# Performance work log

Hardware: AMD Instinct MI355X
Metric: run time of the kernel (lower is better)

The kernel has to match this reference:

```python
import jax, jax.numpy as jnp
import numpy as np

B, CIN, N, K, G, COUT = 8, 128, 2048, 16, 4, 256
NL = COUT // 4          # nl_channels = int(0.25*out_channels) = 64
L = COUT - NL           # l_channels = 192
CL = L // G             # 48 per local head
CNL = NL // G           # 16 per non-local head


def setup_inputs() -> dict:
    key = jax.random.key(0)
    ks = jax.random.split(key, 16)
    s = 0.05
    r = lambda k_, sh: s * jax.random.normal(k_, sh, jnp.float32)
    return {
        "x": jax.random.normal(ks[0], (B, CIN, N, K), jnp.float32),
        "abs_x": jax.random.normal(ks[1], (B, CIN // 2, N, 1), jnp.float32),
        "points": jax.random.normal(ks[2], (B, 3, N), jnp.float32),
        "Wq": r(ks[3], (L, CIN // 2)),
        "Wk": r(ks[4], (L, CIN // 2)),
        "Wv": r(ks[5], (L, CIN)),
        "Wnq": r(ks[6], (NL, CIN // 2)),
        "Wnk": r(ks[7], (NL, CIN // 2)),
        "Wnv1": r(ks[8], (NL, CIN // 2)),
        "Wnv2": r(ks[9], (NL, CIN // 2)),
        "pe_w1": r(ks[10], (3, L)),
        "pe_b1": jnp.zeros((L,), jnp.float32),
        "pe_w2": r(ks[11], (L, L)),
        "pe_b2": jnp.zeros((L,), jnp.float32),
        "npe_w1": r(ks[12], (G, 3, CNL)),
        "npe_b1": jnp.zeros((G, CNL), jnp.float32),
        "npe_w2": r(ks[13], (G, CNL, CNL)),
        "npe_b2": jnp.zeros((G, CNL), jnp.float32),
        "idx": jax.random.randint(ks[14], (B, 1, N, K), 0, N, dtype=jnp.int32),
    }


def _forward(x, abs_x, points, Wq, Wk, Wv, Wnq, Wnk, Wnv1, Wnv2,
             pe_w1, pe_b1, pe_w2, pe_b2, npe_w1, npe_b1, npe_w2, npe_b2, idx):
    b, c, n, k = x.shape
    half = c // 2
    idx_sq = idx[:, 0]                                   # (b,n,k)

    # ---- 1. Local attention over kNN neighbors ----
    lq = jnp.einsum('oc,bcns->bons', Wq, abs_x).reshape(b, G, CL, n, 1)
    lk = jnp.einsum('oc,bcnk->bonk', Wk, x[:, half:] + x[:, :half]).reshape(b, G, CL, n, k)
    lv = jnp.einsum('oc,bcnk->bonk', Wv, x).reshape(b, G, CL, n, k)

    # absolute positional encoding (select_neighbors -> carte MLP)
    nbr = jax.vmap(lambda p, i: p[:, i])(points, idx_sq)  # (b,3,n,k)
    rel = nbr - nbr[..., 0:1]                             # subtract first neighbor
    h = jax.nn.relu(jnp.einsum('bcnk,cd->bnkd', rel, pe_w1) + pe_b1)
    pe = (jnp.einsum('bnkd,de->bnke', h, pe_w2) + pe_b2).transpose(0, 3, 1, 2)
    lk = lk + pe.reshape(b, G, CL, n, k)

    att = jax.nn.softmax((lq * lk).sum(2), axis=-1)       # (b,G,n,k)
    local_feature = jnp.einsum('bgnk,bgcnk->bgcn', att, lv).reshape(b, L, n, 1)

    # ---- scatter-based sparse attention centrality + top-k node selection ----
    idx_flat = idx_sq.reshape(b, n * k)
    att_flat = att.reshape(b, G, n * k)

    def scat(a_g, i):  # a_g: (G, n*k), i: (n*k,)
        return jax.vmap(lambda a: jnp.zeros((n,), a.dtype).at[i].add(a))(a_g)

    cent = jax.vmap(scat)(att_flat, idx_flat)             # (b,G,n)
    vals, inds = jax.lax.top_k(cent, k)                   # (b,G,k)

    # ---- 2. Non-local MHA over selected nodes ----
    a2 = abs_x[..., 0]                                    # (b,half,n)
    nq = jnp.einsum('oc,bcn->bon', Wnq, a2).reshape(b, G, CNL, n)
    nk_ = jnp.einsum('oc,bcn->bon', Wnk, a2).reshape(b, G, CNL, n)
    nv1 = jnp.einsum('oc,bcn->bon', Wnv1, a2).reshape(b, G, CNL, n)
    nv2 = jnp.einsum('oc,bcn->bon', Wnv2, a2).reshape(b, G, CNL, n)

    gi = inds[:, :, None, :]                              # (b,G,1,k)
    nk_sel = jnp.take_along_axis(nk_, gi, axis=3)         # (b,G,CNL,k)
    nv2j = jnp.take_along_axis(nv2, gi, axis=3)           # (b,G,CNL,k)

    # per-group non-local positional encoding (constant over n by construction)
    sel = jnp.take_along_axis(jnp.broadcast_to(points[:, None], (b, G, 3, n)), gi, axis=3)  # (b,G,3,k)
    rel_nl = sel - sel[..., 0:1]
    h2 = jax.nn.relu(jnp.einsum('bgck,gcd->bgkd', rel_nl, npe_w1) + npe_b1[None, :, None, :])
    pe_nl = (jnp.einsum('bgkd,gde->bgke', h2, npe_w2) + npe_b2[None, :, None, :]).transpose(0, 1, 3, 2)  # (b,G,CNL,k)

    att_nl = jax.nn.softmax(jnp.einsum('bgcn,bgck->bgnk', nq, nk_sel + pe_nl), axis=-1)
    # value[b,g,c,n,k] = nv1[...,n] - nv2[...,n] + nv2j[...,k], gated by tanh(centrality)
    w = att_nl * jnp.tanh(vals)[:, :, None, :]            # (b,G,n,k)
    s = w.sum(-1)                                         # (b,G,n)
    nl_feature = (nv1 - nv2) * s[:, :, None, :] + jnp.einsum('bgnk,bgck->bgcn', w, nv2j)
    nl_feature = nl_feature.reshape(b, NL, n, 1)

    return jnp.concatenate([local_feature, nl_feature], axis=1)  # (b,COUT,n,1)


def reference(x, abs_x, points, Wq, Wk, Wv, Wnq, Wnk, Wnv1, Wnv2,
              pe_w1, pe_b1, pe_w2, pe_b2, npe_w1, npe_b1, npe_w2, npe_b2, idx):
    return _forward(x, abs_x, points, Wq, Wk, Wv, Wnq, Wnk, Wnv1, Wnv2,
                    pe_w1, pe_b1, pe_w2, pe_b2, npe_w1, npe_b1, npe_w2, npe_b2, idx)
```

## Files before the change

kernel.cpp:

```cpp
#include <hip/hip_runtime.h>
#include <cstddef>

constexpr int NN = 2048;
constexpr int GG = 4;

__global__ __launch_bounds__(256) void prep_q(const float* __restrict__ Wq,
                                              const float* __restrict__ Wk,
                                              const float* __restrict__ pe_w2,
                                              float* __restrict__ Qbuf) {
    const int g = blockIdx.x >> 6, c2 = blockIdx.x & 63;
    const int row = threadIdx.x;
    float acc = 0.f;
    if (row < 64) {
        for (int j = 0; j < 48; ++j) {
            const int o = g * 48 + j;
            acc = fmaf(Wk[o * 64 + row], Wq[o * 64 + c2], acc);
        }
    } else {
        const int d = row - 64;
        for (int j = 0; j < 48; ++j) {
            const int o = g * 48 + j;
            acc = fmaf(pe_w2[(size_t)d * 192 + o], Wq[o * 64 + c2], acc);
        }
    }
    Qbuf[((size_t)(g * 64 + c2) << 8) + row] = acc;
}

__global__ __launch_bounds__(256, 4) void local_v5(
    const float* __restrict__ x, const float* __restrict__ abs_x,
    const float* __restrict__ points, const float* __restrict__ Wv,
    const float* __restrict__ pe_w1, const float* __restrict__ pe_b1,
    const int* __restrict__ idx, const float* __restrict__ Qbuf,
    float* __restrict__ out, float* __restrict__ cent)
{
    const int bn = blockIdx.x;
    const int b  = bn >> 9;
    const int n0 = (bn & 511) << 2;
    const int tid = threadIdx.x;

    __shared__ int   sidx[64];
    __shared__ float sa2[64][4];
    __shared__ float spts[3][4][16];
    __shared__ float sq[4][4][65];
    __shared__ __align__(16) float s_union[3104];
    __shared__ float spartA[64][17];
    __shared__ float spartB[64][17];
    __shared__ float satt[4][64];

    float* sw  = s_union;
    float* sxw = s_union;

    if (tid < 64) sidx[tid] = idx[((size_t)b * NN + n0) * 16 + tid];
    if (tid < 256) {
        int c = tid >> 2, nl = tid & 3;
        sa2[c][nl] = abs_x[((size_t)b * 64 + c) * NN + n0 + nl];
    }
    __syncthreads();

    if (tid < 192) {
        int c = tid >> 6, r = tid & 63;
        spts[c][r >> 4][r & 15] = points[((size_t)b * 3 + c) * NN + sidx[r]];
    }
    #pragma unroll
    for (int g = 0; g < 4; ++g) {
        const float* qb = Qbuf + ((size_t)g << 14) + tid;
        float a0 = 0.f, a1 = 0.f, a2v = 0.f, a3 = 0.f;
        for (int c2 = 0; c2 < 64; ++c2) {
            const float qv = qb[c2 << 8];
            const float4 av = *(const float4*)&sa2[c2][0];
            a0 = fmaf(qv, av.x, a0); a1 = fmaf(qv, av.y, a1);
            a2v = fmaf(qv, av.z, a2v); a3 = fmaf(qv, av.w, a3);
        }
        if (tid < 64) {
            sq[g][0][tid] = a0; sq[g][1][tid] = a1;
            sq[g][2][tid] = a2v; sq[g][3][tid] = a3;
        } else {
            const int d = tid - 64;
            sw[((g << 2) + 0) * 193 + d] = a0;
            sw[((g << 2) + 1) * 193 + d] = a1;
            sw[((g << 2) + 2) * 193 + d] = a2v;
            sw[((g << 2) + 3) * 193 + d] = a3;
        }
    }
    __syncthreads();

    {
        const int col = tid & 63, ch = tid >> 6;
        const int nl = col >> 4, kk = col & 15;
        const float* xp = x + (((size_t)(b * 128 + ch * 16) * NN) + n0 + nl) * 16 + kk;
        const float* q0 = &sq[0][nl][ch * 16];
        const float* q1 = &sq[1][nl][ch * 16];
        const float* q2 = &sq[2][nl][ch * 16];
        const float* q3 = &sq[3][nl][ch * 16];
        float a0 = 0.f, a1 = 0.f, a2v = 0.f, a3 = 0.f;
        #pragma unroll 4
        for (int i = 0; i < 16; ++i) {
            const float xs = xp[0] + xp[(size_t)64 * NN * 16];
            xp += NN * 16;
            a0 = fmaf(q0[i], xs, a0);
            a1 = fmaf(q1[i], xs, a1);
            a2v = fmaf(q2[i], xs, a2v);
            a3 = fmaf(q3[i], xs, a3);
        }
        spartA[col][ch * 4 + 0] = a0; spartA[col][ch * 4 + 1] = a1;
        spartA[col][ch * 4 + 2] = a2v; spartA[col][ch * 4 + 3] = a3;
    }
    {
        const int col = tid & 63, dh = tid >> 6;
        const int nl = col >> 4, kk = col & 15;
        const float r0 = spts[0][nl][kk] - spts[0][nl][0];
        const float r1 = spts[1][nl][kk] - spts[1][nl][0];
        const float r2 = spts[2][nl][kk] - spts[2][nl][0];
        float p0 = 0.f, p1 = 0.f, p2 = 0.f, p3 = 0.f;
        const int d0 = dh * 48;
        const float* w0 = &sw[((0 << 2) + nl) * 193];
        const float* w1 = &sw[((1 << 2) + nl) * 193];
        const float* w2 = &sw[((2 << 2) + nl) * 193];
        const float* w3 = &sw[((3 << 2) + nl) * 193];
        for (int d = d0; d < d0 + 48; ++d) {
            float h = fmaf(r0, pe_w1[d], fmaf(r1, pe_w1[192 + d], fmaf(r2, pe_w1[384 + d], pe_b1[d])));
            h = fmaxf(h, 0.f);
            p0 = fmaf(h, w0[d], p0);
            p1 = fmaf(h, w1[d], p1);
            p2 = fmaf(h, w2[d], p2);
            p3 = fmaf(h, w3[d], p3);
        }
        spartB[col][dh * 4 + 0] = p0; spartB[col][dh * 4 + 1] = p1;
        spartB[col][dh * 4 + 2] = p2; spartB[col][dh * 4 + 3] = p3;
    }
    __syncthreads();

    float xv[2][16];
    #pragma unroll
    for (int t = 0; t < 2; ++t) {
        const int i2 = t * 256 + tid;
        const int c = i2 >> 2, nl = i2 & 3;
        const float* xp = x + (((size_t)(b * 128 + c) * NN) + n0 + nl) * 16;
        *(float4*)&xv[t][0]  = *(const float4*)(xp);
        *(float4*)&xv[t][4]  = *(const float4*)(xp + 4);
        *(float4*)&xv[t][8]  = *(const float4*)(xp + 8);
        *(float4*)&xv[t][12] = *(const float4*)(xp + 12);
    }

    if (tid < 16) {
        const int g = tid >> 2, nl = tid & 3;
        float lg[16], m = -1e30f;
        #pragma unroll
        for (int kk = 0; kk < 16; ++kk) {
            const int col = nl * 16 + kk;
            lg[kk] = (spartA[col][g] + spartA[col][4 + g] + spartA[col][8 + g] + spartA[col][12 + g])
                   + (spartB[col][g] + spartB[col][4 + g] + spartB[col][8 + g] + spartB[col][12 + g]);
            m = fmaxf(m, lg[kk]);
        }
        float s = 0.f;
        #pragma unroll
        for (int kk = 0; kk < 16; ++kk) { lg[kk] = __expf(lg[kk] - m); s += lg[kk]; }
        const float inv = 1.f / s;
        #pragma unroll
        for (int kk = 0; kk < 16; ++kk) {
            const float a = lg[kk] * inv;
            satt[g][nl * 16 + kk] = a;
            atomicAdd(&cent[((size_t)(b * GG + g) << 11) + sidx[nl * 16 + kk]], a);
        }
    }
    __syncthreads();

    #pragma unroll
    for (int t = 0; t < 2; ++t) {
        const int i2 = t * 256 + tid;
        const int c = i2 >> 2, nl = i2 & 3;
        #pragma unroll
        for (int g = 0; g < 4; ++g) {
            float v = 0.f;
            #pragma unroll
            for (int kk = 0; kk < 16; ++kk) v = fmaf(xv[t][kk], satt[g][nl * 16 + kk], v);
            sxw[(((g << 7) + c) << 2) + nl] = v;
        }
    }
    __syncthreads();

    #pragma unroll
    for (int rep = 0; rep < 3; ++rep) {
        const int i = rep * 256 + tid;
        const int o = i >> 2, nl = i & 3;
        const int g = o / 48;
        const float* wv = Wv + (size_t)o * 128;
        const float* xwp = &sxw[((size_t)(g << 7) << 2) + nl];
        float a = 0.f;
        for (int c = 0; c < 128; c += 4) {
            const float4 w4 = *(const float4*)(wv + c);
            a = fmaf(w4.x, xwp[(c + 0) << 2], a);
            a = fmaf(w4.y, xwp[(c + 1) << 2], a);
            a = fmaf(w4.z, xwp[(c + 2) << 2], a);
            a = fmaf(w4.w, xwp[(c + 3) << 2], a);
        }
        out[(((size_t)b << 8) + o) * NN + n0 + nl] = a;
    }
}

__global__ __launch_bounds__(256) void topk_prep_kernel(
    const float* __restrict__ abs_x, const float* __restrict__ points,
    const float* __restrict__ Wnk, const float* __restrict__ Wnv2,
    const float* __restrict__ npe_w1, const float* __restrict__ npe_b1,
    const float* __restrict__ npe_w2, const float* __restrict__ npe_b2,
    const float* __restrict__ cent,
    float* __restrict__ nkpe, float* __restrict__ nv2j, float* __restrict__ tanhv)
{
    const int bg  = blockIdx.x;
    const int b   = bg >> 2, g = bg & 3;
    const int tid = threadIdx.x;
    __shared__ float sc[2048];
    __shared__ float rv[4];  __shared__ int ri[4];
    __shared__ float svals[16]; __shared__ int sinds[16];
    __shared__ float srel[3][16];
    __shared__ float sh2[16][16];

    for (int i = tid; i < 2048; i += 256) sc[i] = cent[((size_t)bg << 11) + i];
    __syncthreads();
    for (int t = 0; t < 16; ++t) {
        float bv = -1e30f; int bi = 1 << 30;
        for (int i = tid; i < 2048; i += 256) {
            float v = sc[i];
            if (v > bv) { bv = v; bi = i; }
        }
        #pragma unroll
        for (int off = 1; off < 64; off <<= 1) {
            float ov = __shfl_xor(bv, off, 64);
            int   oi = __shfl_xor(bi, off, 64);
            if (ov > bv || (ov == bv && oi < bi)) { bv = ov; bi = oi; }
        }
        if ((tid & 63) == 0) { rv[tid >> 6] = bv; ri[tid >> 6] = bi; }
        __syncthreads();
        if (tid == 0) {
            for (int w = 1; w < 4; ++w)
                if (rv[w] > bv || (rv[w] == bv && ri[w] < bi)) { bv = rv[w]; bi = ri[w]; }
            svals[t] = bv; sinds[t] = bi;
            sc[bi] = -1e30f;
        }
        __syncthreads();
    }

    if (tid < 48) {
        int c = tid >> 4, j = tid & 15;
        srel[c][j] = points[((size_t)b * 3 + c) * NN + sinds[j]]
                   - points[((size_t)b * 3 + c) * NN + sinds[0]];
    }
    __syncthreads();
    {
        int j = tid >> 4, d = tid & 15;
        float a = npe_b1[g * 16 + d];
        #pragma unroll
        for (int c = 0; c < 3; ++c) a = fmaf(srel[c][j], npe_w1[((g * 3 + c) << 4) + d], a);
        sh2[j][d] = fmaxf(a, 0.f);
    }
    __syncthreads();
    {
        int c = tid >> 4, j = tid & 15;
        float a = npe_b2[g * 16 + c];
        #pragma unroll
        for (int d = 0; d < 16; ++d) a = fmaf(sh2[j][d], npe_w2[((g * 16 + d) << 4) + c], a);
        float nk = 0.f, nv = 0.f;
        const int col = sinds[j];
        const float* a2  = abs_x + (size_t)b * 64 * NN + col;
        const float* wkr = Wnk  + ((size_t)(g * 16 + c) << 6);
        const float* wvr = Wnv2 + ((size_t)(g * 16 + c) << 6);
        for (int ci = 0; ci < 64; ++ci) {
            float av = a2[(size_t)ci * NN];
            nk = fmaf(wkr[ci], av, nk);
            nv = fmaf(wvr[ci], av, nv);
        }
        nkpe[((size_t)bg << 8) + (c << 4) + j] = nk + a;
        nv2j[((size_t)bg << 8) + (c << 4) + j] = nv;
    }
    if (tid < 16) tanhv[(bg << 4) + tid] = tanhf(svals[tid]);
}

__global__ __launch_bounds__(256) void nonlocal_kernel(
    const float* __restrict__ abs_x,
    const float* __restrict__ Wnq, const float* __restrict__ Wnv1, const float* __restrict__ Wnv2,
    const float* __restrict__ nkpe, const float* __restrict__ nv2j, const float* __restrict__ tanhv,
    float* __restrict__ out)
{
    const int blk = blockIdx.x;
    const int b   = blk >> 5;
    const int n0  = (blk & 31) << 6;
    const int tid = threadIdx.x;
    const int nl  = tid & 63;
    const int g   = tid >> 6;

    __shared__ float sa2[64][64];
    __shared__ float snkpe[4][16][16];
    __shared__ float snv2j[4][16][16];
    __shared__ float stanh[4][16];

    for (int i = tid; i < 64 * 64; i += 256) {
        int ci = i >> 6, c2 = i & 63;
        sa2[ci][c2] = abs_x[((size_t)b * 64 + ci) * NN + n0 + c2];
    }
    for (int i = tid; i < 1024; i += 256) {
        ((float*)snkpe)[i] = nkpe[((size_t)b << 10) + i];
        ((float*)snv2j)[i] = nv2j[((size_t)b << 10) + i];
    }
    if (tid < 64) ((float*)stanh)[tid] = tanhv[(b << 6) + tid];
    __syncthreads();

    float nq[16], nv1[16], nv2[16];
    #pragma unroll
    for (int c = 0; c < 16; ++c) { nq[c] = 0.f; nv1[c] = 0.f; nv2[c] = 0.f; }
    const float* wq  = Wnq  + (size_t)(g << 4) * 64;
    const float* wv1 = Wnv1 + (size_t)(g << 4) * 64;
    const float* wv2 = Wnv2 + (size_t)(g << 4) * 64;
    for (int ci = 0; ci < 64; ++ci) {
        const float a = sa2[ci][nl];
        #pragma unroll
        for (int c = 0; c < 16; ++c) {
            nq[c]  = fmaf(wq [(c << 6) + ci], a, nq[c]);
            nv1[c] = fmaf(wv1[(c << 6) + ci], a, nv1[c]);
            nv2[c] = fmaf(wv2[(c << 6) + ci], a, nv2[c]);
        }
    }

    float lg[16];
    #pragma unroll
    for (int j = 0; j < 16; ++j) {
        float a = 0.f;
        #pragma unroll
        for (int c = 0; c < 16; ++c) a = fmaf(nq[c], snkpe[g][c][j], a);
        lg[j] = a;
    }
    float m = lg[0];
    #pragma unroll
    for (int j = 1; j < 16; ++j) m = fmaxf(m, lg[j]);
    float s = 0.f;
    float w[16];
    #pragma unroll
    for (int j = 0; j < 16; ++j) { w[j] = __expf(lg[j] - m); s += w[j]; }
    const float inv = 1.f / s;
    float ws = 0.f;
    #pragma unroll
    for (int j = 0; j < 16; ++j) { w[j] = w[j] * inv * stanh[g][j]; ws += w[j]; }
    #pragma unroll
    for (int c = 0; c < 16; ++c) {
        float v = (nv1[c] - nv2[c]) * ws;
        #pragma unroll
        for (int j = 0; j < 16; ++j) v = fmaf(w[j], snv2j[g][c][j], v);
        out[(((size_t)b << 8) + 192 + (g << 4) + c) * NN + n0 + nl] = v;
    }
}

extern "C" void kernel_launch(void* const* d_in, const int* in_sizes, int n_in,
                              void* d_out, int out_size, void* d_ws, size_t ws_size,
                              hipStream_t stream)
{
    (void)in_sizes; (void)n_in; (void)out_size; (void)ws_size;
    const float* x      = (const float*)d_in[0];
    const float* abs_x  = (const float*)d_in[1];
    const float* points = (const float*)d_in[2];
    const float* Wq     = (const float*)d_in[3];
    const float* Wk     = (const float*)d_in[4];
    const float* Wv     = (const float*)d_in[5];
    const float* Wnq    = (const float*)d_in[6];
    const float* Wnk    = (const float*)d_in[7];
    const float* Wnv1   = (const float*)d_in[8];
    const float* Wnv2   = (const float*)d_in[9];
    const float* pe_w1  = (const float*)d_in[10];
    const float* pe_b1  = (const float*)d_in[11];
    const float* pe_w2  = (const float*)d_in[12];
    const float* npe_w1 = (const float*)d_in[14];
    const float* npe_b1 = (const float*)d_in[15];
    const float* npe_w2 = (const float*)d_in[16];
    const float* npe_b2 = (const float*)d_in[17];
    const int*   idx    = (const int*)d_in[18];
    float* out = (float*)d_out;

    float* cent  = (float*)d_ws;
    float* Qbuf  = cent + 65536;
    float* nkpeW = Qbuf + 65536;
    float* nv2jW = nkpeW + 8192;
    float* tanhW = nv2jW + 8192;

    hipMemsetAsync(cent, 0, (size_t)65536 * sizeof(float), stream);
    prep_q<<<256, 256, 0, stream>>>(Wq, Wk, pe_w2, Qbuf);
    local_v5<<<4096, 256, 0, stream>>>(x, abs_x, points, Wv, pe_w1, pe_b1,
                                       idx, Qbuf, out, cent);
    topk_prep_kernel<<<32, 256, 0, stream>>>(abs_x, points, Wnk, Wnv2,
                                             npe_w1, npe_b1, npe_w2, npe_b2,
                                             cent, nkpeW, nv2jW, tanhW);
    nonlocal_kernel<<<8 * 32, 256, 0, stream>>>(abs_x, Wnq, Wnv1, Wnv2,
                                                nkpeW, nv2jW, tanhW, out);
}
```

Before: 248.6 us.

## Precompute per-point folded query weights and process eight points per local block

Adds a separate kernel that multiplies the folded Q matrices by abs_x for every point and writes the result to a large 64 MB workspace buffer. A new local attention kernel then reads these per-point weights instead of recomputing them, and handles eight points per block instead of four. It also computes the weighted x before applying Wv, so the Wv product runs on aggregated values. The new path runs only when the workspace is large enough and otherwise falls back to the old kernel. The risk is the extra global-memory traffic from writing and re-reading the big QW buffer.

Measured after the change: 641.2 us. 158% more time.

```diff
diff --git a/kernel.cpp b/kernel.cpp
--- a/kernel.cpp
+++ b/kernel.cpp
@@ -24,6 +24,192 @@
         }
     }
     Qbuf[((size_t)(g * 64 + c2) << 8) + row] = acc;
+}
+
+__global__ __launch_bounds__(256, 8) void qw_kernel(
+    const float* __restrict__ abs_x, const float* __restrict__ Qbuf,
+    float* __restrict__ QW)
+{
+    const int bt = blockIdx.x;
+    const int b  = bt >> 8;
+    const int n0 = (bt & 255) << 3;
+    const int tid = threadIdx.x;
+    __shared__ float sa2[64][8];
+    for (int i = tid; i < 512; i += 256) {
+        int c = i >> 3, nl = i & 7;
+        sa2[c][nl] = abs_x[((size_t)b * 64 + c) * NN + n0 + nl];
+    }
+    __syncthreads();
+    #pragma unroll
+    for (int g = 0; g < 4; ++g) {
+        const float* qb = Qbuf + ((size_t)g << 14) + tid;
+        float a0 = 0.f, a1 = 0.f, a2v = 0.f, a3 = 0.f, a4 = 0.f, a5 = 0.f, a6 = 0.f, a7 = 0.f;
+        for (int c2 = 0; c2 < 64; ++c2) {
+            const float qv = qb[c2 << 8];
+            const float4 v0 = *(const float4*)&sa2[c2][0];
+            const float4 v1 = *(const float4*)&sa2[c2][4];
+            a0 = fmaf(qv, v0.x, a0); a1 = fmaf(qv, v0.y, a1);
+            a2v = fmaf(qv, v0.z, a2v); a3 = fmaf(qv, v0.w, a3);
+            a4 = fmaf(qv, v1.x, a4); a5 = fmaf(qv, v1.y, a5);
+            a6 = fmaf(qv, v1.z, a6); a7 = fmaf(qv, v1.w, a7);
+        }
+        float* op = QW + (((size_t)(b * NN + n0)) << 10) + (g << 8) + tid;
+        op[0 << 10] = a0;  op[1 << 10] = a1;  op[(size_t)2 << 10] = a2v; op[(size_t)3 << 10] = a3;
+        op[(size_t)4 << 10] = a4; op[(size_t)5 << 10] = a5; op[(size_t)6 << 10] = a6; op[(size_t)7 << 10] = a7;
+    }
+}
+
+__global__ __launch_bounds__(256, 6) void local_v6(
+    const float* __restrict__ x, const float* __restrict__ points,
+    const float* __restrict__ Wv,
+    const float* __restrict__ pe_w1, const float* __restrict__ pe_b1,
+    const int* __restrict__ idx, const float* __restrict__ QW,
+    float* __restrict__ out, float* __restrict__ cent)
+{
+    const int bn = blockIdx.x;
+    const int b  = bn >> 8;
+    const int n0 = (bn & 255) << 3;
+    const int tid = threadIdx.x;
+
+    __shared__ int   sidx[128];
+    __shared__ float spts[3][8][16];
+    __shared__ __align__(16) float s_union[4 * 8 * 132];
+    __shared__ float spart[128][9];
+    __shared__ float satt[8][68];
+
+    float* sq  = s_union;
+    float* sxw = s_union;
+
+    if (tid < 128) sidx[tid] = idx[((size_t)b * NN + n0) * 16 + tid];
+    {
+        const float* qsrc = QW + ((size_t)(b * NN + n0) << 10);
+        #pragma unroll
+        for (int t = 0; t < 8; ++t) {
+            const int i = t * 256 + tid;
+            const int g = i >> 9, nl = (i >> 6) & 7, c2 = i & 63;
+            sq[((g << 3) + nl) * 65 + c2] = qsrc[((size_t)nl << 10) + (g << 8) + c2];
+        }
+    }
+    __syncthreads();
+
+    for (int i = tid; i < 384; i += 256) {
+        int c = i >> 7, r = i & 127;
+        spts[c][r >> 4][r & 15] = points[((size_t)b * 3 + c) * NN + sidx[r]];
+    }
+    __syncthreads();
+
+    {
+        const int col = tid & 127, dh = tid >> 7;
+        const int nl = col >> 4, kk = col & 15;
+        float pA0 = 0.f, pA1 = 0.f, pA2 = 0.f, pA3 = 0.f;
+        {
+            const float* xp = x + (((size_t)(b * 128 + dh * 32) * NN) + n0 + nl) * 16 + kk;
+            const float* q0 = &sq[((0 << 3) + nl) * 65 + dh * 32];
+            const float* q1 = &sq[((1 << 3) + nl) * 65 + dh * 32];
+            const float* q2 = &sq[((2 << 3) + nl) * 65 + dh * 32];
+            const float* q3 = &sq[((3 << 3) + nl) * 65 + dh * 32];
+            for (int i = 0; i < 32; ++i) {
+                const float xs = xp[0] + xp[(size_t)64 * NN * 16];
+                xp += NN * 16;
+                pA0 = fmaf(q0[i], xs, pA0);
+                pA1 = fmaf(q1[i], xs, pA1);
+                pA2 = fmaf(q2[i], xs, pA2);
+                pA3 = fmaf(q3[i], xs, pA3);
+            }
+        }
+        const float r0 = spts[0][nl][kk] - spts[0][nl][0];
+        const float r1 = spts[1][nl][kk] - spts[1][nl][0];
+        const float r2 = spts[2][nl][kk] - spts[2][nl][0];
+        float pB0 = 0.f, pB1 = 0.f, pB2 = 0.f, pB3 = 0.f;
+        const float* wbase = QW + ((size_t)(b * NN + n0 + nl) << 10) + 64;
+        const int d0 = dh * 96;
+        for (int d = d0; d < d0 + 96; d += 4) {
+            const float4 w1a = *(const float4*)&pe_w1[d];
+            const float4 w1b = *(const float4*)&pe_w1[192 + d];
+            const float4 w1c = *(const float4*)&pe_w1[384 + d];
+            const float4 bb  = *(const float4*)&pe_b1[d];
+            const float h0 = fmaxf(fmaf(r0, w1a.x, fmaf(r1, w1b.x, fmaf(r2, w1c.x, bb.x))), 0.f);
+            const float h1 = fmaxf(fmaf(r0, w1a.y, fmaf(r1, w1b.y, fmaf(r2, w1c.y, bb.y))), 0.f);
+            const float h2 = fmaxf(fmaf(r0, w1a.z, fmaf(r1, w1b.z, fmaf(r2, w1c.z, bb.z))), 0.f);
+            const float h3 = fmaxf(fmaf(r0, w1a.w, fmaf(r1, w1b.w, fmaf(r2, w1c.w, bb.w))), 0.f);
+            const float4 wg0 = *(const float4*)&wbase[(0 << 8) + d];
+            const float4 wg1 = *(const float4*)&wbase[(1 << 8) + d];
+            const float4 wg2 = *(const float4*)&wbase[(2 << 8) + d];
+            const float4 wg3 = *(const float4*)&wbase[(3 << 8) + d];
+            pB0 = fmaf(h0, wg0.x, fmaf(h1, wg0.y, fmaf(h2, wg0.z, fmaf(h3, wg0.w, pB0))));
+            pB1 = fmaf(h0, wg1.x, fmaf(h1, wg1.y, fmaf(h2, wg1.z, fmaf(h3, wg1.w, pB1))));
+            pB2 = fmaf(h0, wg2.x, fmaf(h1, wg2.y, fmaf(h2, wg2.z, fmaf(h3, wg2.w, pB2))));
+            pB3 = fmaf(h0, wg3.x, fmaf(h1, wg3.y, fmaf(h2, wg3.z, fmaf(h3, wg3.w, pB3))));
+        }
+        spart[col][dh * 4 + 0] = pA0 + pB0;
+        spart[col][dh * 4 + 1] = pA1 + pB1;
+        spart[col][dh * 4 + 2] = pA2 + pB2;
+        spart[col][dh * 4 + 3] = pA3 + pB3;
+    }
+    __syncthreads();
+
+    if (tid < 32) {
+        const int g = tid >> 3, nl = tid & 7;
+        float lg[16], m = -1e30f;
+        #pragma unroll
+        for (int kk = 0; kk < 16; ++kk) {
+            const int col = nl * 16 + kk;
+            lg[kk] = spart[col][g] + spart[col][4 + g];
+            m = fmaxf(m, lg[kk]);
+        }
+        float s = 0.f;
+        #pragma unroll
+        for (int kk = 0; kk < 16; ++kk) { lg[kk] = __expf(lg[kk] - m); s += lg[kk]; }
+        const float inv = 1.f / s;
+        #pragma unroll
+        for (int kk = 0; kk < 16; ++kk) satt[nl][g * 16 + kk] = lg[kk] * inv;
+    }
+    __syncthreads();
+
+    #pragma unroll
+    for (int t = 0; t < 4; ++t) {
+        const int i2 = t * 256 + tid;
+        const int c = i2 >> 3, nl = i2 & 7;
+        const float* xp = x + (((size_t)(b * 128 + c) * NN) + n0 + nl) * 16;
+        const float4 x0 = *(const float4*)(xp);
+        const float4 x1 = *(const float4*)(xp + 4);
+        const float4 x2 = *(const float4*)(xp + 8);
+        const float4 x3 = *(const float4*)(xp + 12);
+        const float xv[16] = {x0.x, x0.y, x0.z, x0.w, x1.x, x1.y, x1.z, x1.w,
+                              x2.x, x2.y, x2.z, x2.w, x3.x, x3.y, x3.z, x3.w};
+        #pragma unroll
+        for (int g = 0; g < 4; ++g) {
+            float v = 0.f;
+            #pragma unroll
+            for (int kk = 0; kk < 16; ++kk) v = fmaf(xv[kk], satt[nl][g * 16 + kk], v);
+            sxw[((g << 3) + nl) * 132 + c] = v;
+        }
+    }
+    __syncthreads();
+
+    #pragma unroll
+    for (int rep = 0; rep < 6; ++rep) {
+        const int i = rep * 256 + tid;
+        const int o = i >> 3, nl = i & 7;
+        const int g = o / 48;
+        const float* wv  = Wv + (size_t)o * 128;
+        const float* xwp = &sxw[((g << 3) + nl) * 132];
+        float a = 0.f;
+        for (int c = 0; c < 128; c += 4) {
+            const float4 w4  = *(const float4*)(wv + c);
+            const float4 xw4 = *(const float4*)(xwp + c);
+            a = fmaf(w4.x, xw4.x, fmaf(w4.y, xw4.y, fmaf(w4.z, xw4.z, fmaf(w4.w, xw4.w, a))));
+        }
+        out[(((size_t)b << 8) + o) * NN + n0 + nl] = a;
+    }
+
+    if (tid < 32) {
+        const int g = tid >> 3, nl = tid & 7;
+        #pragma unroll
+        for (int kk = 0; kk < 16; ++kk)
+            atomicAdd(&cent[((size_t)(b * GG + g) << 11) + sidx[nl * 16 + kk]],
+                      satt[nl][g * 16 + kk]);
+    }
 }
 
 __global__ __launch_bounds__(256, 4) void local_v5(
@@ -352,7 +538,7 @@
                               void* d_out, int out_size, void* d_ws, size_t ws_size,
                               hipStream_t stream)
 {
-    (void)in_sizes; (void)n_in; (void)out_size; (void)ws_size;
+    (void)in_sizes; (void)n_in; (void)out_size;
     const float* x      = (const float*)d_in[0];
     const float* abs_x  = (const float*)d_in[1];
     const float* points = (const float*)d_in[2];
@@ -378,11 +564,21 @@
     float* nkpeW = Qbuf + 65536;
     float* nv2jW = nkpeW + 8192;
     float* tanhW = nv2jW + 8192;
+    float* QW    = tanhW + 512;
+
+    const size_t need = ((size_t)65536 + 65536 + 8192 + 8192 + 512
+                         + (size_t)8 * 2048 * 1024) * sizeof(float);
 
     hipMemsetAsync(cent, 0, (size_t)65536 * sizeof(float), stream);
     prep_q<<<256, 256, 0, stream>>>(Wq, Wk, pe_w2, Qbuf);
-    local_v5<<<4096, 256, 0, stream>>>(x, abs_x, points, Wv, pe_w1, pe_b1,
-                                       idx, Qbuf, out, cent);
+    if (ws_size >= need) {
+        qw_kernel<<<2048, 256, 0, stream>>>(abs_x, Qbuf, QW);
+        local_v6<<<2048, 256, 0, stream>>>(x, points, Wv, pe_w1, pe_b1,
+                                           idx, QW, out, cent);
+    } else {
+        local_v5<<<4096, 256, 0, stream>>>(x, abs_x, points, Wv, pe_w1, pe_b1,
+                                           idx, Qbuf, out, cent);
+    }
     topk_prep_kernel<<<32, 256, 0, stream>>>(abs_x, points, Wnk, Wnv2,
                                              npe_w1, npe_b1, npe_w2, npe_b2,
                                              cent, nkpeW, nv2jW, tanhW);
```
